# Performance work log

Measured on AMD Instinct MI355X. Metric: run time of the kernel, lower is better.

The kernel has to match this reference:

```python
import jax, jax.numpy as jnp
import numpy as np

N, D, C = 4096, 512, 128
TOPK = 12  # rank-0 hard neg + up to 11 fallback ranks (torch loop breaks at loop_cnt>=10 -> max rank 11)


def setup_inputs() -> dict:
    key = jax.random.key(0)
    k1, k2, k3, k4, k5 = jax.random.split(key, 5)
    return {
        "inputs": jax.random.normal(k1, (N, D), jnp.float32),
        "prediction": jax.random.normal(k2, (N, C), jnp.float32),
        "targets": jax.random.randint(k3, (N,), 0, C),
        "true_targets": jax.random.randint(k4, (N,), 0, C),
        "prob": jax.random.uniform(k5, (N,), jnp.float32),
        "threshold": jnp.float32(0.5),
    }


def _gumbel_argmax(key, mask):
    # uniform random choice over True entries of each row (Gumbel-max trick)
    g = jax.random.gumbel(key, mask.shape, jnp.float32)
    return jnp.argmax(jnp.where(mask, g, -jnp.inf), axis=1)


def reference(inputs, prediction, targets, true_targets, prob, threshold):
    margin = jnp.float32(0.3)
    n = inputs.shape[0]
    rows = jnp.arange(n)
    # pairwise euclidean distance: ||xi||^2 + ||xj||^2 - 2 xi.xj, clamp+sqrt
    sq = jnp.sum(inputs * inputs, axis=1)
    d2 = sq[:, None] + sq[None, :] - 2.0 * (inputs @ inputs.T)
    dist = jnp.sqrt(jnp.clip(d2, 1e-12))  # [n, n]

    eye = jnp.eye(n, dtype=bool)
    same = targets[:, None] == targets[None, :]
    is_neg = ~same
    conf = prob >= threshold  # is_confident per anchor

    key = jax.random.key(42)
    kp, kp2 = jax.random.split(key)

    # random positive (!= i) and hardest negative per row
    ap_idx = _gumbel_argmax(kp, same & ~eye)
    neg_dist = jnp.where(is_neg, dist, jnp.inf)
    an_idx = jnp.argmin(neg_dist, axis=1)

    ap0 = dist[rows, ap_idx]
    an0 = dist[rows, an_idx]
    pos_conf = prob[ap_idx] >= threshold
    neg_conf = prob[an_idx] >= threshold
    # false-negative test: hard neg predicted as anchor's (noisy) label
    is_fn = jnp.argmax(prediction[an_idx], axis=1) == targets

    # case B (pos conf, neg unconf, FN): walk ranked negs for first confident one (ranks 1..11)
    nv, ni = jax.lax.top_k(-neg_dist, TOPK)  # smallest TOPK neg distances
    cand_conf = prob[ni] >= threshold
    tail = cand_conf[:, 1:]
    found = jnp.any(tail, axis=1)
    r = jnp.where(found, 1 + jnp.argmax(tail, axis=1), TOPK - 1)
    an_B = dist[rows, ni[rows, r]]

    # cases C / D-notFN: resample a confident positive (!= i); fallback to original pos
    conf_pos = same & ~eye & (prob >= threshold)[None, :]
    new_pos = jnp.where(jnp.any(conf_pos, axis=1), _gumbel_argmax(kp2, conf_pos), ap_idx)
    ap_new = dist[rows, new_pos]

    caseB = pos_conf & ~neg_conf & is_fn
    swap = (~pos_conf) & (neg_conf | ~is_fn)  # case C or case D-notFN
    inverse = (~pos_conf) & (~neg_conf) & is_fn

    half = (ap0 + an0) * 0.5
    ap = jnp.where(caseB, half, jnp.where(swap, ap_new, ap0))
    an = jnp.where(caseB, an_B, jnp.where(swap, half, an0))

    row_loss = jnp.where(inverse,
                         jax.nn.relu(an - ap + margin),
                         jax.nn.relu(ap - an + margin))
    cnt = jnp.sum(conf)
    loss = jnp.sum(jnp.where(conf, row_loss, 0.0)) / jnp.maximum(cnt, 1).astype(jnp.float32)
    correct = jnp.sum((an >= ap) & conf)
    return loss, correct
```

## Files before the change

### kernel.cpp

```cpp
#include <hip/hip_runtime.h>
#include <stdint.h>
#include <math.h>

#define N_ 4096
#define D_ 512
#define C_ 128

typedef __attribute__((ext_vector_type(8))) short bf16x8;
typedef __attribute__((ext_vector_type(4))) float f32x4;

__host__ __device__ __forceinline__ uint32_t rotl32_(uint32_t x, int d) {
  return (x << d) | (x >> (32 - d));
}
__host__ __device__ inline void tf2x32(uint32_t k0, uint32_t k1,
                                       uint32_t x0, uint32_t x1,
                                       uint32_t& y0, uint32_t& y1) {
  const uint32_t k2 = k0 ^ k1 ^ 0x1BD11BDAu;
#define TF_R(rr) { x0 += x1; x1 = rotl32_(x1, rr); x1 ^= x0; }
  x0 += k0; x1 += k1;
  TF_R(13) TF_R(15) TF_R(26) TF_R(6)
  x0 += k1; x1 += k2 + 1u;
  TF_R(17) TF_R(29) TF_R(16) TF_R(24)
  x0 += k2; x1 += k0 + 2u;
  TF_R(13) TF_R(15) TF_R(26) TF_R(6)
  x0 += k0; x1 += k1 + 3u;
  TF_R(17) TF_R(29) TF_R(16) TF_R(24)
  x0 += k1; x1 += k2 + 4u;
  TF_R(13) TF_R(15) TF_R(26) TF_R(6)
  x0 += k2; x1 += k0 + 5u;
#undef TF_R
  y0 = x0; y1 = x1;
}

__device__ __forceinline__ float gumbel_ij(uint32_t k0, uint32_t k1, uint32_t m) {
  uint32_t y0, y1;
  tf2x32(k0, k1, 0u, m, y0, y1);
  uint32_t bits = y0 ^ y1;
  uint32_t vb = (bits >> 9) | 0x3f800000u;
  float f = __uint_as_float(vb) - 1.0f;
  float u = (f == 0.0f) ? 1.1754943508222875e-38f : f;
  return -logf(-logf(u));
}

__device__ __forceinline__ unsigned short f2bf(float x) {
  unsigned int b = __float_as_uint(x);
  b += 0x7fffu + ((b >> 16) & 1u);
  return (unsigned short)(b >> 16);
}
__device__ __forceinline__ float bf2f(unsigned short u) {
  return __uint_as_float(((unsigned int)u) << 16);
}

__device__ __forceinline__ void gll16(const void* g, void* lds) {
  __builtin_amdgcn_global_load_lds(
      (const __attribute__((address_space(1))) unsigned int*)g,
      (__attribute__((address_space(3))) unsigned int*)lds, 16, 0, 0);
}

__global__ __launch_bounds__(64) void prep_k(const float* __restrict__ inputs,
                                             const float* __restrict__ pred,
                                             float* __restrict__ sq,
                                             int* __restrict__ pam,
                                             float* __restrict__ accum,
                                             unsigned short* __restrict__ XH,
                                             unsigned short* __restrict__ XL,
                                             int do_split) {
  int i = blockIdx.x;
  int lane = threadIdx.x;
  if (i == 0 && lane == 0) {
    accum[0] = 0.0f;
    ((unsigned*)accum)[1] = 0u;
    ((unsigned*)accum)[2] = 0u;
  }
  const float4* rp = (const float4*)(inputs + (size_t)i * D_);
  float s = 0.0f;
#pragma unroll
  for (int q = 0; q < 2; ++q) {
    float4 v = rp[lane + 64 * q];
    s += v.x * v.x + v.y * v.y + v.z * v.z + v.w * v.w;
    if (do_split) {
      unsigned short h0 = f2bf(v.x), h1 = f2bf(v.y), h2 = f2bf(v.z), h3 = f2bf(v.w);
      unsigned short g0 = f2bf(v.x - bf2f(h0)), g1 = f2bf(v.y - bf2f(h1));
      unsigned short g2 = f2bf(v.z - bf2f(h2)), g3 = f2bf(v.w - bf2f(h3));
      uint2 hp, lp;
      hp.x = (unsigned)h0 | ((unsigned)h1 << 16); hp.y = (unsigned)h2 | ((unsigned)h3 << 16);
      lp.x = (unsigned)g0 | ((unsigned)g1 << 16); lp.y = (unsigned)g2 | ((unsigned)g3 << 16);
      *(uint2*)&XH[(size_t)i * D_ + 4 * (lane + 64 * q)] = hp;
      *(uint2*)&XL[(size_t)i * D_ + 4 * (lane + 64 * q)] = lp;
    }
  }
#pragma unroll
  for (int off = 32; off; off >>= 1) s += __shfl_down(s, off);
  if (lane == 0) sq[i] = s;

  float v0 = pred[(size_t)i * C_ + lane];
  float v1 = pred[(size_t)i * C_ + 64 + lane];
  float bv; int bi;
  if (v1 > v0) { bv = v1; bi = lane + 64; } else { bv = v0; bi = lane; }
#pragma unroll
  for (int off = 32; off; off >>= 1) {
    float ov = __shfl_down(bv, off);
    int oi = __shfl_down(bi, off);
    if (ov > bv || (ov == bv && oi < bi)) { bv = ov; bi = oi; }
  }
  if (lane == 0) pam[i] = bi;
}

__global__ __launch_bounds__(256, 2) void bigk2_k(const unsigned short* __restrict__ XH,
                                                  const unsigned short* __restrict__ XL,
                                                  const int* __restrict__ targets,
                                                  const float* __restrict__ sq,
                                                  float* __restrict__ pD,
                                                  int* __restrict__ pI) {
  __shared__ float U[18432];
  __shared__ float sqc[512];
  __shared__ int tcs[512];
  __shared__ float sqr[64];
  __shared__ int trs[64];

  short* AH = (short*)U;
  short* AL = (short*)(U + 1024);
  short* BH = (short*)(U + 2048);
  short* BL = (short*)(U + 10240);
  float* Dl = U;
  float* MD = U + 9216;
  int* MI = (int*)(U + 12288);

  const int tid = threadIdx.x, w = tid >> 6, l = tid & 63;
  const int rb = blockIdx.x >> 3, sl = blockIdx.x & 7;
  const int rbase = rb * 64, cbase0 = sl * 512;

  sqc[tid] = sq[cbase0 + tid]; sqc[tid + 256] = sq[cbase0 + 256 + tid];
  tcs[tid] = targets[cbase0 + tid]; tcs[tid + 256] = targets[cbase0 + 256 + tid];
  if (tid < 64) { sqr[tid] = sq[rbase + tid]; trs[tid] = targets[rbase + tid]; }

  const int lr = l & 15, lk = (l >> 4) * 8;
  const size_t aoff = (size_t)(rbase + w * 16 + lr) * D_ + lk;
  const size_t boff0 = (size_t)(cbase0 + (w * 8) * 16 + lr) * D_ + lk;

  f32x4 acc[4][8];
#pragma unroll
  for (int rt = 0; rt < 4; ++rt)
#pragma unroll
    for (int c = 0; c < 8; ++c) acc[rt][c] = (f32x4){0.f, 0.f, 0.f, 0.f};

  for (int kc = 0; kc < 16; ++kc) {
    const int kb = kc * 32;
    __syncthreads();
    gll16(XH + aoff + kb, AH + w * 512);
    gll16(XL + aoff + kb, AL + w * 512);
#pragma unroll
    for (int c = 0; c < 8; ++c) {
      gll16(XH + boff0 + (size_t)c * 16 * D_ + kb, BH + (w * 8 + c) * 512);
      gll16(XL + boff0 + (size_t)c * 16 * D_ + kb, BL + (w * 8 + c) * 512);
    }
    __syncthreads();

    bf16x8 ah[4], am[4];
#pragma unroll
    for (int rt = 0; rt < 4; ++rt) {
      ah[rt] = *(const bf16x8*)(AH + rt * 512 + l * 8);
      am[rt] = *(const bf16x8*)(AL + rt * 512 + l * 8);
    }
#pragma unroll
    for (int c = 0; c < 8; ++c) {
      bf16x8 bh = *(const bf16x8*)(BH + (w * 8 + c) * 512 + l * 8);
      bf16x8 bl = *(const bf16x8*)(BL + (w * 8 + c) * 512 + l * 8);
#pragma unroll
      for (int rt = 0; rt < 4; ++rt) {
        acc[rt][c] = __builtin_amdgcn_mfma_f32_16x16x32_bf16(ah[rt], bh, acc[rt][c], 0, 0, 0);
        acc[rt][c] = __builtin_amdgcn_mfma_f32_16x16x32_bf16(ah[rt], bl, acc[rt][c], 0, 0, 0);
        acc[rt][c] = __builtin_amdgcn_mfma_f32_16x16x32_bf16(am[rt], bh, acc[rt][c], 0, 0, 0);
      }
    }
  }

  float dl[12]; int il[12];
#pragma unroll
  for (int q = 0; q < 12; ++q) { dl[q] = INFINITY; il[q] = 0; }
  const int srow = tid >> 2, scq = tid & 3;
  const int orow = (l >> 4) * 4;

  for (int g = 0; g < 4; ++g) {
    __syncthreads();
    if (w == g) {
#pragma unroll
      for (int rt = 0; rt < 4; ++rt)
#pragma unroll
        for (int c = 0; c < 8; ++c)
#pragma unroll
          for (int r = 0; r < 4; ++r) {
            int row = rt * 16 + orow + r;
            int cl = c * 16 + lr;
            float d2 = sqr[row] + sqc[g * 128 + cl] - 2.0f * acc[rt][c][r];
            float d = (trs[row] == tcs[g * 128 + cl]) ? INFINITY : sqrtf(fmaxf(d2, 1e-12f));
            Dl[row * 133 + cl] = d;
          }
    }
    __syncthreads();
    for (int q = 0; q < 32; ++q) {
      float d = Dl[srow * 133 + scq + 4 * q];
      if (d < dl[11]) {
        int col = cbase0 + g * 128 + scq + 4 * q;
        bool placed = false;
#pragma unroll
        for (int t = 11; t >= 1; --t) {
          if (!placed) {
            if (dl[t - 1] > d) { dl[t] = dl[t - 1]; il[t] = il[t - 1]; }
            else { dl[t] = d; il[t] = col; placed = true; }
          }
        }
        if (!placed) { dl[0] = d; il[0] = col; }
      }
    }
  }

#pragma unroll
  for (int q = 0; q < 12; ++q) { MD[tid * 12 + q] = dl[q]; MI[tid * 12 + q] = il[q]; }
  __syncthreads();
  if ((tid & 3) == 0) {
    int row = tid >> 2;
    int grow = rbase + row;
    float* outD = pD + ((size_t)grow * 8 + sl) * 12;
    int* outI = pI + ((size_t)grow * 8 + sl) * 12;
    int p0 = 0, p1 = 0, p2 = 0, p3 = 0;
    for (int o = 0; o < 12; ++o) {
      float bd = INFINITY; int bi = 0x7fffffff; int bc = 0;
      if (p0 < 12) { float d = MD[(row * 4 + 0) * 12 + p0]; int ix = MI[(row * 4 + 0) * 12 + p0]; if (d < bd || (d == bd && ix < bi)) { bd = d; bi = ix; bc = 0; } }
      if (p1 < 12) { float d = MD[(row * 4 + 1) * 12 + p1]; int ix = MI[(row * 4 + 1) * 12 + p1]; if (d < bd || (d == bd && ix < bi)) { bd = d; bi = ix; bc = 1; } }
      if (p2 < 12) { float d = MD[(row * 4 + 2) * 12 + p2]; int ix = MI[(row * 4 + 2) * 12 + p2]; if (d < bd || (d == bd && ix < bi)) { bd = d; bi = ix; bc = 2; } }
      if (p3 < 12) { float d = MD[(row * 4 + 3) * 12 + p3]; int ix = MI[(row * 4 + 3) * 12 + p3]; if (d < bd || (d == bd && ix < bi)) { bd = d; bi = ix; bc = 3; } }
      outD[o] = bd; outI[o] = bi;
      if (bc == 0) p0++; else if (bc == 1) p1++; else if (bc == 2) p2++; else p3++;
    }
  }
}

__global__ __launch_bounds__(256, 2) void bigk_k(const float* __restrict__ inputs,
                                                 const int* __restrict__ targets,
                                                 const float* __restrict__ sq,
                                                 float* __restrict__ pD,
                                                 int* __restrict__ pI) {
  __shared__ float U[10496];
  __shared__ float sqc[256];
  __shared__ int tcs[256];
  __shared__ float sqr[64];
  __shared__ int trs[64];

  float* Al = U;
  float* Bl = U + 2176;
  float* Dl = U;
  float* MD = U;
  int* MI = (int*)(U + 3072);

  const int tid = threadIdx.x;
  const int rb = blockIdx.x >> 3, sl = blockIdx.x & 7;
  const int rbase = rb * 64, cbase0 = sl * 512;

  if (tid < 64) { sqr[tid] = sq[rbase + tid]; trs[tid] = targets[rbase + tid]; }

  float dl[12]; int il[12];
#pragma unroll
  for (int q = 0; q < 12; ++q) { dl[q] = INFINITY; il[q] = 0; }

  const int w = tid >> 6, lane = tid & 63;
  const int rg = lane >> 3, cg = lane & 7;
  const int r0 = rg * 8, c0l = w * 64 + cg * 8;
  const int srow = tid >> 2, scq = tid & 3;

  for (int ci = 0; ci < 2; ++ci) {
    const int cbase = cbase0 + ci * 256;
    __syncthreads();
    sqc[tid] = sq[cbase + tid];
    tcs[tid] = targets[cbase + tid];

    float acc[8][8];
#pragma unroll
    for (int a = 0; a < 8; ++a)
#pragma unroll
      for (int b = 0; b < 8; ++b) acc[a][b] = 0.0f;

    for (int kc = 0; kc < 16; ++kc) {
      const int kb = kc * 32;
      __syncthreads();
#pragma unroll
      for (int q = 0; q < 2; ++q) {
        int idx = tid + 256 * q;
        int row = idx >> 3, kq = idx & 7;
        float4 v = *(const float4*)(inputs + (size_t)(rbase + row) * D_ + kb + kq * 4);
        Al[(4 * kq + 0) * 68 + row] = v.x;
        Al[(4 * kq + 1) * 68 + row] = v.y;
        Al[(4 * kq + 2) * 68 + row] = v.z;
        Al[(4 * kq + 3) * 68 + row] = v.w;
      }
#pragma unroll
      for (int q = 0; q < 8; ++q) {
        int idx = tid + 256 * q;
        int col = idx >> 3, kq = idx & 7;
        float4 v = *(const float4*)(inputs + (size_t)(cbase + col) * D_ + kb + kq * 4);
        Bl[(4 * kq + 0) * 260 + col] = v.x;
        Bl[(4 * kq + 1) * 260 + col] = v.y;
        Bl[(4 * kq + 2) * 260 + col] = v.z;
        Bl[(4 * kq + 3) * 260 + col] = v.w;
      }
      __syncthreads();
#pragma unroll 4
      for (int k = 0; k < 32; ++k) {
        float4 a0 = *(const float4*)&Al[k * 68 + r0];
        float4 a1 = *(const float4*)&Al[k * 68 + r0 + 4];
        float4 b0 = *(const float4*)&Bl[k * 260 + c0l];
        float4 b1 = *(const float4*)&Bl[k * 260 + c0l + 4];
        float a_[8] = {a0.x, a0.y, a0.z, a0.w, a1.x, a1.y, a1.z, a1.w};
        float b_[8] = {b0.x, b0.y, b0.z, b0.w, b1.x, b1.y, b1.z, b1.w};
#pragma unroll
        for (int ii = 0; ii < 8; ++ii)
#pragma unroll
          for (int jj = 0; jj < 8; ++jj)
            acc[ii][jj] = fmaf(a_[ii], b_[jj], acc[ii][jj]);
      }
    }

    for (int h = 0; h < 2; ++h) {
      __syncthreads();
#pragma unroll
      for (int i = 0; i < 8; ++i) {
        float si = sqr[r0 + i];
        int ti_ = trs[r0 + i];
#pragma unroll
        for (int jj = 0; jj < 4; ++jj) {
          int j = 4 * h + jj;
          float d2 = si + sqc[c0l + j] - 2.0f * acc[i][j];
          float d = (ti_ == tcs[c0l + j]) ? INFINITY : sqrtf(fmaxf(d2, 1e-12f));
          Dl[(r0 + i) * 129 + (w * 32 + cg * 4 + jj)] = d;
        }
      }
      __syncthreads();
      for (int q = 0; q < 32; ++q) {
        float d = Dl[srow * 129 + scq * 32 + q];
        if (d < dl[11]) {
          int u = scq * 32 + q;
          int col = cbase + ((u >> 5) << 6) + (((u >> 2) & 7) << 3) + (h << 2) + (u & 3);
          bool placed = false;
#pragma unroll
          for (int t = 11; t >= 1; --t) {
            if (!placed) {
              if (dl[t - 1] > d) { dl[t] = dl[t - 1]; il[t] = il[t - 1]; }
              else { dl[t] = d; il[t] = col; placed = true; }
            }
          }
          if (!placed) { dl[0] = d; il[0] = col; }
        }
      }
    }
  }

  __syncthreads();
#pragma unroll
  for (int q = 0; q < 12; ++q) { MD[tid * 12 + q] = dl[q]; MI[tid * 12 + q] = il[q]; }
  __syncthreads();
  if ((tid & 3) == 0) {
    int row = tid >> 2;
    int grow = rbase + row;
    float* outD = pD + ((size_t)grow * 8 + sl) * 12;
    int* outI = pI + ((size_t)grow * 8 + sl) * 12;
    int p0 = 0, p1 = 0, p2 = 0, p3 = 0;
    for (int o = 0; o < 12; ++o) {
      float bd = INFINITY; int bi = 0x7fffffff; int bc = 0;
      if (p0 < 12) { float d = MD[(row * 4 + 0) * 12 + p0]; int ix = MI[(row * 4 + 0) * 12 + p0]; if (d < bd || (d == bd && ix < bi)) { bd = d; bi = ix; bc = 0; } }
      if (p1 < 12) { float d = MD[(row * 4 + 1) * 12 + p1]; int ix = MI[(row * 4 + 1) * 12 + p1]; if (d < bd || (d == bd && ix < bi)) { bd = d; bi = ix; bc = 1; } }
      if (p2 < 12) { float d = MD[(row * 4 + 2) * 12 + p2]; int ix = MI[(row * 4 + 2) * 12 + p2]; if (d < bd || (d == bd && ix < bi)) { bd = d; bi = ix; bc = 2; } }
      if (p3 < 12) { float d = MD[(row * 4 + 3) * 12 + p3]; int ix = MI[(row * 4 + 3) * 12 + p3]; if (d < bd || (d == bd && ix < bi)) { bd = d; bi = ix; bc = 3; } }
      outD[o] = bd; outI[o] = bi;
      if (bc == 0) p0++; else if (bc == 1) p1++; else if (bc == 2) p2++; else p3++;
    }
  }
}

__device__ __forceinline__ float wdist2(float4 xi0, float4 xi1,
                                        const float* __restrict__ inputs,
                                        const float* __restrict__ sq,
                                        int i, int j, int lane) {
  const float4* b = (const float4*)(inputs + (size_t)j * D_);
  float4 y0 = b[lane], y1 = b[lane + 64];
  float s = xi0.x * y0.x + xi0.y * y0.y + xi0.z * y0.z + xi0.w * y0.w +
            xi1.x * y1.x + xi1.y * y1.y + xi1.z * y1.z + xi1.w * y1.w;
#pragma unroll
  for (int off = 32; off; off >>= 1) s += __shfl_xor(s, off);
  float d2 = sq[i] + sq[j] - 2.0f * s;
  return sqrtf(fmaxf(d2, 1e-12f));
}

__global__ __launch_bounds__(256) void finalize_k(const float* __restrict__ inputs,
                                                  const int* __restrict__ targets,
                                                  const float* __restrict__ prob,
                                                  const float* __restrict__ thr_p,
                                                  const float* __restrict__ sq,
                                                  const int* __restrict__ pam,
                                                  const float* __restrict__ pD,
                                                  const int* __restrict__ pI,
                                                  float* __restrict__ accum,
                                                  uint32_t kp0, uint32_t kp1,
                                                  uint32_t kq0, uint32_t kq1) {
  const int wid = threadIdx.x >> 6, lane = threadIdx.x & 63;
  const int i = blockIdx.x * 4 + wid;
  const float thr = *thr_p;
  const int ti = targets[i];

  float g1 = -INFINITY; int i1 = 0;
  float g2 = -INFINITY; int i2 = 0;
  int f2 = 0;
  for (int j = lane; j < N_; j += 64) {
    if (targets[j] == ti && j != i) {
      uint32_t m = ((uint32_t)i << 12) | (uint32_t)j;
      float g = gumbel_ij(kp0, kp1, m);
      if (g > g1 || (g == g1 && j < i1)) { g1 = g; i1 = j; }
      if (prob[j] >= thr) {
        float gg = gumbel_ij(kq0, kq1, m);
        if (gg > g2 || (gg == g2 && j < i2)) { g2 = gg; i2 = j; }
        f2 = 1;
      }
    }
  }
#pragma unroll
  for (int off = 32; off; off >>= 1) {
    float og = __shfl_xor(g1, off); int oi = __shfl_xor(i1, off);
    if (og > g1 || (og == g1 && oi < i1)) { g1 = og; i1 = oi; }
    float oh = __shfl_xor(g2, off); int oj = __shfl_xor(i2, off);
    if (oh > g2 || (oh == g2 && oj < i2)) { g2 = oh; i2 = oj; }
  }
  f2 = __any(f2);
  const int ap_idx = i1;
  const int new_pos = f2 ? i2 : ap_idx;

  const float4* arow = (const float4*)(inputs + (size_t)i * D_);
  float4 xi0 = arow[lane], xi1 = arow[lane + 64];
  const float ap0 = wdist2(xi0, xi1, inputs, sq, i, ap_idx, lane);
  const float ap_new = wdist2(xi0, xi1, inputs, sq, i, new_pos, lane);

  const float* rowD = pD + (size_t)i * 96;
  const int* rowI = pI + (size_t)i * 96;
  int ci_[12];
  {
    int p0 = 0, p1 = 0, p2 = 0, p3 = 0, p4 = 0, p5 = 0, p6 = 0, p7 = 0;
#pragma unroll
    for (int o = 0; o < 12; ++o) {
      float bd = INFINITY; int bi = 0x7fffffff; int bs = 0;
#define HEADQ(s, ps) if (ps < 12) { float d = rowD[(s) * 12 + ps]; int ix = rowI[(s) * 12 + ps]; if (d < bd || (d == bd && ix < bi)) { bd = d; bi = ix; bs = (s); } }
      HEADQ(0, p0) HEADQ(1, p1) HEADQ(2, p2) HEADQ(3, p3)
      HEADQ(4, p4) HEADQ(5, p5) HEADQ(6, p6) HEADQ(7, p7)
#undef HEADQ
      ci_[o] = bi;
      if (bs == 0) p0++; else if (bs == 1) p1++; else if (bs == 2) p2++; else if (bs == 3) p3++;
      else if (bs == 4) p4++; else if (bs == 5) p5++; else if (bs == 6) p6++; else p7++;
    }
  }
  float de[12];
#pragma unroll
  for (int o = 0; o < 12; ++o) de[o] = wdist2(xi0, xi1, inputs, sq, i, ci_[o], lane);

  float an0 = de[0]; int an_idx = ci_[0]; int minpos = 0;
#pragma unroll
  for (int o = 1; o < 12; ++o)
    if (de[o] < an0 || (de[o] == an0 && ci_[o] < an_idx)) { an0 = de[o]; an_idx = ci_[o]; minpos = o; }
  float anB = INFINITY; int anBi = 0x7fffffff; bool fB = false;
#pragma unroll
  for (int o = 0; o < 12; ++o) {
    if (o != minpos) {
      bool cf = prob[ci_[o]] >= thr;
      if (cf && (de[o] < anB || (de[o] == anB && ci_[o] < anBi))) { anB = de[o]; anBi = ci_[o]; fB = true; }
    }
  }
  if (!fB) {
    anB = de[0]; anBi = ci_[0];
#pragma unroll
    for (int o = 1; o < 12; ++o)
      if (de[o] > anB || (de[o] == anB && ci_[o] > anBi)) { anB = de[o]; anBi = ci_[o]; }
  }
  const float an_B = anB;

  if (lane == 0) {
    bool neg_conf = prob[an_idx] >= thr;
    bool pos_conf = prob[ap_idx] >= thr;
    bool is_fn = (pam[an_idx] == ti);
    bool caseB = pos_conf && !neg_conf && is_fn;
    bool swap_ = !pos_conf && (neg_conf || !is_fn);
    bool inverse = !pos_conf && !neg_conf && is_fn;
    float half = 0.5f * (ap0 + an0);
    float ap = caseB ? half : (swap_ ? ap_new : ap0);
    float an = caseB ? an_B : (swap_ ? half : an0);
    const float margin = 0.3f;
    float rl = inverse ? fmaxf(an - ap + margin, 0.0f) : fmaxf(ap - an + margin, 0.0f);
    bool conf_i = prob[i] >= thr;
    if (conf_i) {
      atomicAdd(&accum[0], rl);
      atomicAdd(((unsigned*)accum) + 2, 1u);
      if (an >= ap) atomicAdd(((unsigned*)accum) + 1, 1u);
    }
  }
}

__global__ void writeout_k(const float* __restrict__ accum, float* __restrict__ out) {
  unsigned correct = ((const unsigned*)accum)[1];
  unsigned cnt = ((const unsigned*)accum)[2];
  out[0] = accum[0] / fmaxf((float)cnt, 1.0f);
  out[1] = (float)correct;
}

extern "C" void kernel_launch(void* const* d_in, const int* in_sizes, int n_in,
                              void* d_out, int out_size, void* d_ws, size_t ws_size,
                              hipStream_t stream) {
  const float* inputs = (const float*)d_in[0];
  const float* pred = (const float*)d_in[1];
  const int* targets = (const int*)d_in[2];
  const float* prob = (const float*)d_in[4];
  const float* thr = (const float*)d_in[5];
  float* out = (float*)d_out;

  float* sq = (float*)d_ws;
  int* pam = (int*)d_ws + N_;
  float* pD = (float*)d_ws + 2 * N_;
  int* pI = (int*)d_ws + 2 * N_ + N_ * 96;
  float* accum = (float*)d_ws + 2 * N_ + 2 * (N_ * 96);
  const size_t split_off = (size_t)(2 * N_ + 2 * (N_ * 96) + 16) * 4;
  unsigned short* XH = (unsigned short*)((char*)d_ws + split_off);
  unsigned short* XL = XH + (size_t)N_ * D_;
  const size_t need = split_off + (size_t)2 * N_ * D_ * 2;
  const int use_v2 = (ws_size >= need) ? 1 : 0;

  uint32_t kp0, kp1, kq0, kq1;
  tf2x32(0u, 42u, 0u, 0u, kp0, kp1);
  tf2x32(0u, 42u, 0u, 1u, kq0, kq1);

  prep_k<<<dim3(N_), dim3(64), 0, stream>>>(inputs, pred, sq, pam, accum, XH, XL, use_v2);
  if (use_v2)
    bigk2_k<<<dim3(512), dim3(256), 0, stream>>>(XH, XL, targets, sq, pD, pI);
  else
    bigk_k<<<dim3(512), dim3(256), 0, stream>>>(inputs, targets, sq, pD, pI);
  finalize_k<<<dim3(N_ / 4), dim3(256), 0, stream>>>(inputs, targets, prob, thr, sq, pam,
                                                     pD, pI, accum, kp0, kp1, kq0, kq1);
  writeout_k<<<dim3(1), dim3(1), 0, stream>>>(accum, out);
}
```

Before: 352.9 us.

## Bucket rows by class for positive sampling and load GEMM operands directly

During prep, each row is appended to a per-class index list through an atomic counter. The finalize kernel then runs its Gumbel sampling of positives over only the same-class list, instead of scanning all N targets for every anchor. The distance GEMM kernel stops staging bf16 hi/lo tiles through LDS and loads MFMA operands straight from global memory into registers. This removes the per-k-chunk barriers but means every wave reloads the A tiles redundantly. LDS is shrunk and reused for the distance and merge buffers, and the row padding changes from 133 to 132, which may raise bank conflicts. Class lists are capped at 256 entries, so a class larger than that would be truncated.

```diff
diff --git a/kernel.cpp b/kernel.cpp
--- a/kernel.cpp
+++ b/kernel.cpp
@@ -5,6 +5,7 @@
 #define N_ 4096
 #define D_ 512
 #define C_ 128
+#define MAXC 256
 
 typedef __attribute__((ext_vector_type(8))) short bf16x8;
 typedef __attribute__((ext_vector_type(4))) float f32x4;
@@ -57,21 +58,28 @@
       (__attribute__((address_space(3))) unsigned int*)lds, 16, 0, 0);
 }
 
-__global__ __launch_bounds__(64) void prep_k(const float* __restrict__ inputs,
-                                             const float* __restrict__ pred,
-                                             float* __restrict__ sq,
-                                             int* __restrict__ pam,
-                                             float* __restrict__ accum,
-                                             unsigned short* __restrict__ XH,
-                                             unsigned short* __restrict__ XL,
-                                             int do_split) {
-  int i = blockIdx.x;
-  int lane = threadIdx.x;
-  if (i == 0 && lane == 0) {
+__global__ void zero_k(float* __restrict__ accum, int* __restrict__ ccnt) {
+  int t = threadIdx.x;
+  if (t == 0) {
     accum[0] = 0.0f;
     ((unsigned*)accum)[1] = 0u;
     ((unsigned*)accum)[2] = 0u;
   }
+  if (t < C_) ccnt[t] = 0;
+}
+
+__global__ __launch_bounds__(64) void prep_k(const float* __restrict__ inputs,
+                                             const float* __restrict__ pred,
+                                             const int* __restrict__ targets,
+                                             float* __restrict__ sq,
+                                             int* __restrict__ pam,
+                                             int* __restrict__ ccnt,
+                                             int* __restrict__ clist,
+                                             unsigned short* __restrict__ XH,
+                                             unsigned short* __restrict__ XL,
+                                             int do_split, int do_list) {
+  int i = blockIdx.x;
+  int lane = threadIdx.x;
   const float4* rp = (const float4*)(inputs + (size_t)i * D_);
   float s = 0.0f;
 #pragma unroll
@@ -103,29 +111,28 @@
     int oi = __shfl_down(bi, off);
     if (ov > bv || (ov == bv && oi < bi)) { bv = ov; bi = oi; }
   }
-  if (lane == 0) pam[i] = bi;
-}
-
-__global__ __launch_bounds__(256, 2) void bigk2_k(const unsigned short* __restrict__ XH,
+  if (lane == 0) {
+    pam[i] = bi;
+    if (do_list) {
+      int t = targets[i];
+      int p = atomicAdd(&ccnt[t], 1);
+      if (p < MAXC) clist[t * MAXC + p] = i;
+    }
+  }
+}
+
+__global__ __launch_bounds__(256, 2) void bigk3_k(const unsigned short* __restrict__ XH,
                                                   const unsigned short* __restrict__ XL,
                                                   const int* __restrict__ targets,
                                                   const float* __restrict__ sq,
                                                   float* __restrict__ pD,
                                                   int* __restrict__ pI) {
-  __shared__ float U[18432];
+  __shared__ float U[8448];
   __shared__ float sqc[512];
   __shared__ int tcs[512];
   __shared__ float sqr[64];
   __shared__ int trs[64];
 
-  short* AH = (short*)U;
-  short* AL = (short*)(U + 1024);
-  short* BH = (short*)(U + 2048);
-  short* BL = (short*)(U + 10240);
-  float* Dl = U;
-  float* MD = U + 9216;
-  int* MI = (int*)(U + 12288);
-
   const int tid = threadIdx.x, w = tid >> 6, l = tid & 63;
   const int rb = blockIdx.x >> 3, sl = blockIdx.x & 7;
   const int rbase = rb * 64, cbase0 = sl * 512;
@@ -135,8 +142,18 @@
   if (tid < 64) { sqr[tid] = sq[rbase + tid]; trs[tid] = targets[rbase + tid]; }
 
   const int lr = l & 15, lk = (l >> 4) * 8;
-  const size_t aoff = (size_t)(rbase + w * 16 + lr) * D_ + lk;
-  const size_t boff0 = (size_t)(cbase0 + (w * 8) * 16 + lr) * D_ + lk;
+  const unsigned short* aH[4]; const unsigned short* aL[4];
+  const unsigned short* bH[8]; const unsigned short* bL[8];
+#pragma unroll
+  for (int rt = 0; rt < 4; ++rt) {
+    size_t o = (size_t)(rbase + rt * 16 + lr) * D_ + lk;
+    aH[rt] = XH + o; aL[rt] = XL + o;
+  }
+#pragma unroll
+  for (int c = 0; c < 8; ++c) {
+    size_t o = (size_t)(cbase0 + (w * 8 + c) * 16 + lr) * D_ + lk;
+    bH[c] = XH + o; bL[c] = XL + o;
+  }
 
   f32x4 acc[4][8];
 #pragma unroll
@@ -146,35 +163,26 @@
 
   for (int kc = 0; kc < 16; ++kc) {
     const int kb = kc * 32;
-    __syncthreads();
-    gll16(XH + aoff + kb, AH + w * 512);
-    gll16(XL + aoff + kb, AL + w * 512);
+    bf16x8 ah[4], al_[4];
+#pragma unroll
+    for (int rt = 0; rt < 4; ++rt) {
+      ah[rt] = *(const bf16x8*)(aH[rt] + kb);
+      al_[rt] = *(const bf16x8*)(aL[rt] + kb);
+    }
 #pragma unroll
     for (int c = 0; c < 8; ++c) {
-      gll16(XH + boff0 + (size_t)c * 16 * D_ + kb, BH + (w * 8 + c) * 512);
-      gll16(XL + boff0 + (size_t)c * 16 * D_ + kb, BL + (w * 8 + c) * 512);
-    }
-    __syncthreads();
-
-    bf16x8 ah[4], am[4];
-#pragma unroll
-    for (int rt = 0; rt < 4; ++rt) {
-      ah[rt] = *(const bf16x8*)(AH + rt * 512 + l * 8);
-      am[rt] = *(const bf16x8*)(AL + rt * 512 + l * 8);
-    }
-#pragma unroll
-    for (int c = 0; c < 8; ++c) {
-      bf16x8 bh = *(const bf16x8*)(BH + (w * 8 + c) * 512 + l * 8);
-      bf16x8 bl = *(const bf16x8*)(BL + (w * 8 + c) * 512 + l * 8);
+      bf16x8 bh = *(const bf16x8*)(bH[c] + kb);
+      bf16x8 bl = *(const bf16x8*)(bL[c] + kb);
 #pragma unroll
       for (int rt = 0; rt < 4; ++rt) {
         acc[rt][c] = __builtin_amdgcn_mfma_f32_16x16x32_bf16(ah[rt], bh, acc[rt][c], 0, 0, 0);
         acc[rt][c] = __builtin_amdgcn_mfma_f32_16x16x32_bf16(ah[rt], bl, acc[rt][c], 0, 0, 0);
-        acc[rt][c] = __builtin_amdgcn_mfma_f32_16x16x32_bf16(am[rt], bh, acc[rt][c], 0, 0, 0);
-      }
-    }
-  }
-
+        acc[rt][c] = __builtin_amdgcn_mfma_f32_16x16x32_bf16(al_[rt], bh, acc[rt][c], 0, 0, 0);
+      }
+    }
+  }
+
+  float* Dl = U;
   float dl[12]; int il[12];
 #pragma unroll
   for (int q = 0; q < 12; ++q) { dl[q] = INFINITY; il[q] = 0; }
@@ -194,12 +202,12 @@
             int cl = c * 16 + lr;
             float d2 = sqr[row] + sqc[g * 128 + cl] - 2.0f * acc[rt][c][r];
             float d = (trs[row] == tcs[g * 128 + cl]) ? INFINITY : sqrtf(fmaxf(d2, 1e-12f));
-            Dl[row * 133 + cl] = d;
+            Dl[row * 132 + cl] = d;
           }
     }
     __syncthreads();
     for (int q = 0; q < 32; ++q) {
-      float d = Dl[srow * 133 + scq + 4 * q];
+      float d = Dl[srow * 132 + scq + 4 * q];
       if (d < dl[11]) {
         int col = cbase0 + g * 128 + scq + 4 * q;
         bool placed = false;
@@ -215,6 +223,9 @@
     }
   }
 
+  __syncthreads();
+  float* MD = U;
+  int* MI = (int*)(U + 3072);
 #pragma unroll
   for (int q = 0; q < 12; ++q) { MD[tid * 12 + q] = dl[q]; MI[tid * 12 + q] = il[q]; }
   __syncthreads();
@@ -398,9 +409,12 @@
                                                   const int* __restrict__ pam,
                                                   const float* __restrict__ pD,
                                                   const int* __restrict__ pI,
+                                                  const int* __restrict__ ccnt,
+                                                  const int* __restrict__ clist,
                                                   float* __restrict__ accum,
                                                   uint32_t kp0, uint32_t kp1,
-                                                  uint32_t kq0, uint32_t kq1) {
+                                                  uint32_t kq0, uint32_t kq1,
+                                                  int use_list) {
   const int wid = threadIdx.x >> 6, lane = threadIdx.x & 63;
   const int i = blockIdx.x * 4 + wid;
   const float thr = *thr_p;
@@ -409,15 +423,36 @@
   float g1 = -INFINITY; int i1 = 0;
   float g2 = -INFINITY; int i2 = 0;
   int f2 = 0;
-  for (int j = lane; j < N_; j += 64) {
-    if (targets[j] == ti && j != i) {
-      uint32_t m = ((uint32_t)i << 12) | (uint32_t)j;
-      float g = gumbel_ij(kp0, kp1, m);
-      if (g > g1 || (g == g1 && j < i1)) { g1 = g; i1 = j; }
-      if (prob[j] >= thr) {
-        float gg = gumbel_ij(kq0, kq1, m);
-        if (gg > g2 || (gg == g2 && j < i2)) { g2 = gg; i2 = j; }
-        f2 = 1;
+  if (use_list) {
+    int cnt = ccnt[ti]; if (cnt > MAXC) cnt = MAXC;
+    const int* lst = clist + (size_t)ti * MAXC;
+    for (int base = 0; base < cnt; base += 64) {
+      int idx = base + lane;
+      if (idx < cnt) {
+        int j = lst[idx];
+        if (j != i) {
+          uint32_t m = ((uint32_t)i << 12) | (uint32_t)j;
+          float g = gumbel_ij(kp0, kp1, m);
+          if (g > g1 || (g == g1 && j < i1)) { g1 = g; i1 = j; }
+          if (prob[j] >= thr) {
+            float gg = gumbel_ij(kq0, kq1, m);
+            if (gg > g2 || (gg == g2 && j < i2)) { g2 = gg; i2 = j; }
+            f2 = 1;
+          }
+        }
+      }
+    }
+  } else {
+    for (int j = lane; j < N_; j += 64) {
+      if (targets[j] == ti && j != i) {
+        uint32_t m = ((uint32_t)i << 12) | (uint32_t)j;
+        float g = gumbel_ij(kp0, kp1, m);
+        if (g > g1 || (g == g1 && j < i1)) { g1 = g; i1 = j; }
+        if (prob[j] >= thr) {
+          float gg = gumbel_ij(kq0, kq1, m);
+          if (gg > g2 || (gg == g2 && j < i2)) { g2 = gg; i2 = j; }
+          f2 = 1;
+        }
       }
     }
   }
@@ -521,7 +556,10 @@
   float* pD = (float*)d_ws + 2 * N_;
   int* pI = (int*)d_ws + 2 * N_ + N_ * 96;
   float* accum = (float*)d_ws + 2 * N_ + 2 * (N_ * 96);
-  const size_t split_off = (size_t)(2 * N_ + 2 * (N_ * 96) + 16) * 4;
+  int* ccnt = (int*)accum + 16;
+  int* clist = ccnt + C_;
+  const size_t base_f = (size_t)(2 * N_ + 2 * (N_ * 96) + 16 + C_ + C_ * MAXC);
+  const size_t split_off = ((base_f * 4 + 15) / 16) * 16;
   unsigned short* XH = (unsigned short*)((char*)d_ws + split_off);
   unsigned short* XL = XH + (size_t)N_ * D_;
   const size_t need = split_off + (size_t)2 * N_ * D_ * 2;
@@ -531,12 +569,15 @@
   tf2x32(0u, 42u, 0u, 0u, kp0, kp1);
   tf2x32(0u, 42u, 0u, 1u, kq0, kq1);
 
-  prep_k<<<dim3(N_), dim3(64), 0, stream>>>(inputs, pred, sq, pam, accum, XH, XL, use_v2);
+  zero_k<<<dim3(1), dim3(128), 0, stream>>>(accum, ccnt);
+  prep_k<<<dim3(N_), dim3(64), 0, stream>>>(inputs, pred, targets, sq, pam, ccnt, clist,
+                                            XH, XL, use_v2, use_v2);
   if (use_v2)
-    bigk2_k<<<dim3(512), dim3(256), 0, stream>>>(XH, XL, targets, sq, pD, pI);
+    bigk3_k<<<dim3(512), dim3(256), 0, stream>>>(XH, XL, targets, sq, pD, pI);
   else
     bigk_k<<<dim3(512), dim3(256), 0, stream>>>(inputs, targets, sq, pD, pI);
   finalize_k<<<dim3(N_ / 4), dim3(256), 0, stream>>>(inputs, targets, prob, thr, sq, pam,
-                                                     pD, pI, accum, kp0, kp1, kq0, kq1);
+                                                     pD, pI, ccnt, clist, accum,
+                                                     kp0, kp1, kq0, kq1, use_v2);
   writeout_k<<<dim3(1), dim3(1), 0, stream>>>(accum, out);
 }
```

Result: slower. 403.9 us (+14.5%).
